# Optimization experiments

Measured on AMD Instinct MI355X. Metric: run time of the kernel, lower is better.

## Reference

```python
import jax, jax.numpy as jnp
import numpy as np

B, N, D, H = 4, 2048, 1024, 16
HD = D // H          # head dim before LRPE doubling
CHUNK = 64
BASE = 10000.0
EPS = 1e-6


def setup_inputs() -> dict:
    key = jax.random.key(0)
    ks = jax.random.split(key, 8)
    s = 0.02
    return {
        "x": jax.random.normal(ks[0], (B, N, D), jnp.float32),
        "Wq": jax.random.normal(ks[1], (D, D), jnp.float32) * s,
        "Wk": jax.random.normal(ks[2], (D, D), jnp.float32) * s,
        "Wv": jax.random.normal(ks[3], (D, D), jnp.float32) * s,
        "Wo": jax.random.normal(ks[4], (D, D), jnp.float32) * s,
        "Wg1": jax.random.normal(ks[5], (D, H), jnp.float32) * s,
        "Wg2": jax.random.normal(ks[6], (H, D), jnp.float32) * s,
        "norm_w": jnp.ones((D,), jnp.float32),
    }


def _lrpe(x, theta):
    # cosine LRPE (lrpe_type=6): d -> 2d, concat([x*cos, x*sin])
    c = jnp.cos(theta)[None, :, None, :]
    s = jnp.sin(theta)[None, :, None, :]
    return jnp.concatenate([x * c, x * s], axis=-1)


def _chunk_gla(q, k, v, g):
    # GLA chunked scan: S_t = diag(exp(g_t)) S_{t-1} + k_t^T v_t ; o_t = q_t S_t
    # q,k,g: (b,n,h,dk), v: (b,n,h,dv)
    b, n, h, dk = q.shape
    dv = v.shape[-1]
    nc = n // CHUNK

    def to_chunks(t):
        return t.reshape(b, nc, CHUNK, t.shape[2], t.shape[3]).transpose(1, 0, 2, 3, 4)

    qc, kc, vc, gc = map(to_chunks, (q, k, v, g))  # (nc,b,C,h,*)
    mask = jnp.tril(jnp.ones((CHUNK, CHUNK), bool))

    def step(S, inp):
        qi, ki, vi, gi = inp                      # (b,C,h,dk/dv)
        G = jnp.cumsum(gi, axis=1)                # inclusive cumsum of log decay
        q_g = qi * jnp.exp(G)
        k_g = ki * jnp.exp(-G)
        o_inter = jnp.einsum('bchk,bhkv->bchv', q_g, S)
        A = jnp.einsum('bchk,bshk->bhcs', q_g, k_g)
        A = jnp.where(mask[None, None], A, 0.0)
        o_intra = jnp.einsum('bhcs,bshv->bchv', A, vi)
        G_last = G[:, -1:]                        # (b,1,h,dk)
        S = S * jnp.exp(G_last[:, 0])[..., None] + jnp.einsum(
            'bchk,bchv->bhkv', ki * jnp.exp(G_last - G), vi)
        return S, o_inter + o_intra

    S0 = jnp.zeros((b, h, dk, dv), q.dtype)
    _, o = jax.lax.scan(step, S0, (qc, kc, vc, gc))
    return o.transpose(1, 0, 2, 3, 4).reshape(b, n, h, dv)


def reference(x, Wq, Wk, Wv, Wo, Wg1, Wg2, norm_w):
    b, n, d = x.shape
    q = jax.nn.silu(x @ Wq).reshape(b, n, H, HD)
    k_raw = (x @ Wk).reshape(b, n, H, HD)
    v = (x @ Wv).reshape(b, n, H, HD)

    # log-space cumulative decay from raw k projection (scalar_decay=False path)
    f = jnp.concatenate([jnp.zeros((b, 1, H, HD), jnp.float32),
                         k_raw.astype(jnp.float32)], axis=1)
    z = jax.lax.cumlogsumexp(f, axis=1)           # (b,n+1,H,HD)
    log_f = z[:, :-1] - z[:, 1:]                  # per-step log decay (<=0)
    k = jnp.exp(k_raw - z[:, 1:])                 # normalized keys

    # cosine LRPE: angles (n,HD), doubles head dim
    theta = jnp.arange(n, dtype=jnp.float32)[:, None] * \
        (BASE ** (-2.0 * jnp.arange(HD, dtype=jnp.float32) / HD))[None]
    q = _lrpe(q, theta)
    k = _lrpe(k, theta)
    g = jnp.concatenate([log_f, log_f], axis=-1)  # repeat '... d -> ... (2 d)'

    o = _chunk_gla(q, k, v, g)                    # (b,n,H,HD)
    o = o.reshape(b, n, d)

    gate = jax.nn.sigmoid((x @ Wg1) @ Wg2)        # low-rank output gate
    o = o * gate
    o = o * jax.lax.rsqrt(jnp.mean(o * o, axis=-1, keepdims=True) + EPS) * norm_w
    return o @ Wo
```

## Files before the change

kernel.cpp:

```cpp
#include <hip/hip_runtime.h>
#include <hip/hip_bf16.h>
#include <math.h>

#define B_ 4
#define N_ 2048
#define D_ 1024
#define H_ 16
#define HD_ 64

typedef __attribute__((ext_vector_type(8))) short bf16x8;
typedef __attribute__((ext_vector_type(8))) unsigned short u16x8;
typedef __attribute__((ext_vector_type(4))) float f32x4;

#define AS1(p) ((const __attribute__((address_space(1))) void*)(p))
#define AS3(p) ((__attribute__((address_space(3))) void*)(p))

__device__ inline float bf2f(unsigned short u) { return __uint_as_float(((unsigned)u) << 16); }
__device__ inline unsigned short f2bf(float f) {
  unsigned u = __float_as_uint(f);
  return (unsigned short)((u + 0x7fffu + ((u >> 16) & 1u)) >> 16);
}
__device__ inline unsigned short f2h(float f) {
  _Float16 h = (_Float16)f; unsigned short u; __builtin_memcpy(&u, &h, 2); return u;
}
__device__ inline float h2f(unsigned short u) {
  _Float16 h; __builtin_memcpy(&h, &u, 2); return (float)h;
}
__device__ inline float lseop_fast(float a, float b) {
  float mx = fmaxf(a, b), mn = fminf(a, b);
  return mx + __logf(1.f + __expf(mn - mx));
}

__global__ __launch_bounds__(256) void cast_x_bf16(const float* __restrict__ x,
                                                   unsigned short* __restrict__ xb) {
  const int t = blockIdx.x * 256 + threadIdx.x;
  float4 a = ((const float4*)x)[(size_t)t * 2];
  float4 b = ((const float4*)x)[(size_t)t * 2 + 1];
  union { unsigned short u[8]; uint4 q; } pk;
  pk.u[0] = f2bf(a.x); pk.u[1] = f2bf(a.y); pk.u[2] = f2bf(a.z); pk.u[3] = f2bf(a.w);
  pk.u[4] = f2bf(b.x); pk.u[5] = f2bf(b.y); pk.u[6] = f2bf(b.z); pk.u[7] = f2bf(b.w);
  ((uint4*)xb)[t] = pk.q;
}

__global__ __launch_bounds__(256) void cast_w_all(
    const float* __restrict__ Wq, const float* __restrict__ Wk,
    const float* __restrict__ Wv, const float* __restrict__ Wo,
    unsigned short* __restrict__ Wqkv_p, unsigned short* __restrict__ Wo_p) {
  const int bid = blockIdx.x;
  const int which = bid >> 9;
  const float* W = (which == 0) ? Wq : (which == 1) ? Wk : (which == 2) ? Wv : Wo;
  const int col0 = (which == 1) ? 1024 : (which == 2) ? 2048 : 0;
  const int Ntot = (which == 3) ? 1024 : 3072;
  unsigned short* dst = (which == 3) ? Wo_p : Wqkv_p;
  const int t = (bid & 511) * 256 + threadIdx.x;
  const int kg = t >> 10, n = t & 1023;
  union { unsigned short u[8]; uint4 q; } pk;
#pragma unroll
  for (int r = 0; r < 8; ++r)
    pk.u[r] = f2bf(W[(size_t)(kg * 8 + r) * 1024 + n]);
  *(uint4*)&dst[((size_t)kg * Ntot + col0 + n) * 8] = pk.q;
}

__global__ __launch_bounds__(256) void pack_wg1(const float* __restrict__ Wg1,
                                                unsigned short* __restrict__ Wp) {
  const int t = blockIdx.x * 256 + threadIdx.x;
  const int kg = t >> 4, hh = t & 15;
  union { unsigned short us[8]; u16x8 v; } pk;
#pragma unroll
  for (int r = 0; r < 8; ++r)
    pk.us[r] = f2bf(Wg1[(size_t)(kg * 8 + r) * 16 + hh]);
  *(u16x8*)&Wp[((size_t)kg * 16 + hh) * 8] = pk.v;
}

__global__ __launch_bounds__(256) void gate_logits(
    const unsigned short* __restrict__ x_bf, const unsigned short* __restrict__ Wg1p,
    float* __restrict__ tg) {
  __shared__ unsigned short Wl[128 * 16 * 8];
  const int tid = threadIdx.x;
  const int lane = tid & 63, w = tid >> 6;
  const int lr = lane & 15, lg = lane >> 4;
#pragma unroll
  for (int u = 0; u < 8; ++u) {
    const int flat = u * 256 + tid;
    *(u16x8*)&Wl[flat * 8] = *(const u16x8*)&Wg1p[(size_t)flat * 8];
  }
  __syncthreads();
  const int row = blockIdx.x * 64 + w * 16 + lr;
  f32x4 acc = (f32x4){0.f, 0.f, 0.f, 0.f};
  for (int ks = 0; ks < 32; ++ks) {
    bf16x8 a = *(const bf16x8*)&x_bf[(size_t)row * 1024 + ks * 32 + lg * 8];
    bf16x8 b = *(const bf16x8*)&Wl[((ks * 4 + lg) * 16 + lr) * 8];
    acc = __builtin_amdgcn_mfma_f32_16x16x32_bf16(a, b, acc, 0, 0, 0);
  }
  const int orow = blockIdx.x * 64 + w * 16 + 4 * lg;
#pragma unroll
  for (int reg = 0; reg < 4; ++reg)
    tg[(size_t)(orow + reg) * 16 + lr] = acc[reg];
}

__global__ __launch_bounds__(256) void rope_fill(float* __restrict__ ropeT) {
  const int t = blockIdx.x * 256 + threadIdx.x;
  const int n = t >> 6, hd = t & 63;
  const float freq = expf((float)hd * -0.28782313662425575f);
  float s, c;
  sincosf((float)n * freq, &s, &c);
  ropeT[(size_t)n * 128 + hd] = c;
  ropeT[(size_t)n * 128 + 64 + hd] = s;
}

__global__ __launch_bounds__(256) void gemm_qkv(
    const unsigned short* __restrict__ A, const unsigned short* __restrict__ Wp,
    unsigned short* __restrict__ qb, unsigned short* __restrict__ kh,
    unsigned short* __restrict__ vb, float* __restrict__ T, int M, int K) {
  const int Nn = 3072;
  __shared__ unsigned short Asm[2][128 * 32];
  __shared__ unsigned short Bsm[2][4 * 128 * 8];

  const int tid = threadIdx.x;
  const int lane = tid & 63;
  const int w = tid >> 6;
  const int nb = Nn >> 7;
  const int nwg = gridDim.x;
  const int cpx = nwg >> 3;
  int bid = blockIdx.x;
  bid = (bid & 7) * cpx + (bid >> 3);
  const int by = bid / nb, bx = bid % nb;
  const int m0 = by * 128, n0 = bx * 128;
  const int wr = w >> 1, wc = w & 1;

  f32x4 acc[4][4];
#pragma unroll
  for (int i = 0; i < 4; ++i)
#pragma unroll
    for (int j = 0; j < 4; ++j) acc[i][j] = (f32x4){0.f, 0.f, 0.f, 0.f};

  const int rA0 = w * 16 + (lane >> 2);
  const int rA1 = (w + 4) * 16 + (lane >> 2);
  const int sA0 = (lane & 3) ^ ((rA0 >> 1) & 3);
  const int sA1 = (lane & 3) ^ ((rA1 >> 1) & 3);
  const unsigned short* gA0 = A + (size_t)(m0 + rA0) * K + sA0 * 8;
  const unsigned short* gA1 = A + (size_t)(m0 + rA1) * K + sA1 * 8;
  const unsigned short* gB0 = Wp + (size_t)(w >> 1) * Nn * 8 +
                              (size_t)(n0 + (w & 1) * 64 + lane) * 8;
  const unsigned short* gB1 = Wp + (size_t)((w + 4) >> 1) * Nn * 8 +
                              (size_t)(n0 + ((w + 4) & 1) * 64 + lane) * 8;

  int offA[4], offB[4];
#pragma unroll
  for (int m = 0; m < 4; ++m) {
    const int rowf = wr * 64 + m * 16 + (lane & 15);
    const int sp = (lane >> 4) ^ ((rowf >> 1) & 3);
    offA[m] = rowf * 32 + sp * 8;
  }
#pragma unroll
  for (int n = 0; n < 4; ++n) {
    const int colf = wc * 64 + n * 16 + (lane & 15);
    offB[n] = (lane >> 4) * 1024 + colf * 8;
  }

  auto STAGE = [&](int buf, int t) {
    const int kt = t * 32;
    const size_t kB = (size_t)(kt >> 3) * Nn * 8;
    __builtin_amdgcn_global_load_lds(AS1(gA0 + kt), AS3(&Asm[buf][w * 512]), 16, 0, 0);
    __builtin_amdgcn_global_load_lds(AS1(gA1 + kt), AS3(&Asm[buf][(w + 4) * 512]), 16, 0, 0);
    __builtin_amdgcn_global_load_lds(AS1(gB0 + kB), AS3(&Bsm[buf][w * 512]), 16, 0, 0);
    __builtin_amdgcn_global_load_lds(AS1(gB1 + kB), AS3(&Bsm[buf][(w + 4) * 512]), 16, 0, 0);
  };

  const int NT = K >> 5;
  STAGE(0, 0);
  __syncthreads();
  int cur = 0;
  for (int t = 0; t < NT; ++t) {
    if (t + 1 < NT) STAGE(cur ^ 1, t + 1);
    bf16x8 af[4], bfr[4];
#pragma unroll
    for (int m = 0; m < 4; ++m) af[m] = *(const bf16x8*)&Asm[cur][offA[m]];
#pragma unroll
    for (int n = 0; n < 4; ++n) bfr[n] = *(const bf16x8*)&Bsm[cur][offB[n]];
#pragma unroll
    for (int m = 0; m < 4; ++m)
#pragma unroll
      for (int n = 0; n < 4; ++n)
        acc[m][n] = __builtin_amdgcn_mfma_f32_16x16x32_bf16(af[m], bfr[n], acc[m][n], 0, 0, 0);
    __syncthreads();
    cur ^= 1;
  }

  const int crow = (lane >> 4) * 4;
  const int ccol = lane & 15;
  const int slice = bx >> 3;
  if (slice == 1) {
#pragma unroll
    for (int n = 0; n < 4; ++n) {
      float se = 0.f;
#pragma unroll
      for (int m = 0; m < 4; ++m)
#pragma unroll
        for (int r = 0; r < 4; ++r) {
          float vv = acc[m][n][r];
          se += __expf(vv);
          kh[(size_t)(m0 + wr * 64 + m * 16 + crow + r) * 1024 +
             (n0 & 1023) + wc * 64 + n * 16 + ccol] = f2h(vv);
        }
      se += __shfl_xor(se, 16);
      se += __shfl_xor(se, 32);
      if ((lane >> 4) == 0) {
        const int bb = m0 >> 11;
        const int h = ((n0 & 1023) + wc * 64) >> 6;
        const int hd = n * 16 + ccol;
        const int c = ((m0 & 2047) >> 6) + wr;
        T[(size_t)((bb * 16 + h) * 64 + hd) * 32 + c] = __logf(se);
      }
    }
  } else {
#pragma unroll
    for (int m = 0; m < 4; ++m)
#pragma unroll
      for (int n = 0; n < 4; ++n)
#pragma unroll
        for (int r = 0; r < 4; ++r) {
          float vv = acc[m][n][r];
          const size_t idx = (size_t)(m0 + wr * 64 + m * 16 + crow + r) * 1024 +
                             (n0 & 1023) + wc * 64 + n * 16 + ccol;
          if (slice == 0) {
            vv = vv / (1.f + __expf(-vv));
            qb[idx] = f2bf(vv);
          } else {
            vb[idx] = f2bf(vv);
          }
        }
  }
}

__global__ __launch_bounds__(256) void gemm_bf16(
    const unsigned short* __restrict__ A, const unsigned short* __restrict__ Wp,
    float* __restrict__ Cf, int M, int K, int Nn) {
  __shared__ unsigned short Asm[2][128 * 32];
  __shared__ unsigned short Bsm[2][4 * 128 * 8];

  const int tid = threadIdx.x;
  const int lane = tid & 63;
  const int w = tid >> 6;
  const int nb = Nn >> 7;
  const int nwg = gridDim.x;
  const int cpx = nwg >> 3;
  int bid = blockIdx.x;
  bid = (bid & 7) * cpx + (bid >> 3);
  const int by = bid / nb, bx = bid % nb;
  const int m0 = by * 128, n0 = bx * 128;
  const int wr = w >> 1, wc = w & 1;

  f32x4 acc[4][4];
#pragma unroll
  for (int i = 0; i < 4; ++i)
#pragma unroll
    for (int j = 0; j < 4; ++j) acc[i][j] = (f32x4){0.f, 0.f, 0.f, 0.f};

  const int rA0 = w * 16 + (lane >> 2);
  const int rA1 = (w + 4) * 16 + (lane >> 2);
  const int sA0 = (lane & 3) ^ ((rA0 >> 1) & 3);
  const int sA1 = (lane & 3) ^ ((rA1 >> 1) & 3);
  const unsigned short* gA0 = A + (size_t)(m0 + rA0) * K + sA0 * 8;
  const unsigned short* gA1 = A + (size_t)(m0 + rA1) * K + sA1 * 8;
  const unsigned short* gB0 = Wp + (size_t)(w >> 1) * Nn * 8 +
                              (size_t)(n0 + (w & 1) * 64 + lane) * 8;
  const unsigned short* gB1 = Wp + (size_t)((w + 4) >> 1) * Nn * 8 +
                              (size_t)(n0 + ((w + 4) & 1) * 64 + lane) * 8;

  int offA[4], offB[4];
#pragma unroll
  for (int m = 0; m < 4; ++m) {
    const int rowf = wr * 64 + m * 16 + (lane & 15);
    const int sp = (lane >> 4) ^ ((rowf >> 1) & 3);
    offA[m] = rowf * 32 + sp * 8;
  }
#pragma unroll
  for (int n = 0; n < 4; ++n) {
    const int colf = wc * 64 + n * 16 + (lane & 15);
    offB[n] = (lane >> 4) * 1024 + colf * 8;
  }

  auto STAGE = [&](int buf, int t) {
    const int kt = t * 32;
    const size_t kB = (size_t)(kt >> 3) * Nn * 8;
    __builtin_amdgcn_global_load_lds(AS1(gA0 + kt), AS3(&Asm[buf][w * 512]), 16, 0, 0);
    __builtin_amdgcn_global_load_lds(AS1(gA1 + kt), AS3(&Asm[buf][(w + 4) * 512]), 16, 0, 0);
    __builtin_amdgcn_global_load_lds(AS1(gB0 + kB), AS3(&Bsm[buf][w * 512]), 16, 0, 0);
    __builtin_amdgcn_global_load_lds(AS1(gB1 + kB), AS3(&Bsm[buf][(w + 4) * 512]), 16, 0, 0);
  };

  const int NT = K >> 5;
  STAGE(0, 0);
  __syncthreads();
  int cur = 0;
  for (int t = 0; t < NT; ++t) {
    if (t + 1 < NT) STAGE(cur ^ 1, t + 1);
    bf16x8 af[4], bfr[4];
#pragma unroll
    for (int m = 0; m < 4; ++m) af[m] = *(const bf16x8*)&Asm[cur][offA[m]];
#pragma unroll
    for (int n = 0; n < 4; ++n) bfr[n] = *(const bf16x8*)&Bsm[cur][offB[n]];
#pragma unroll
    for (int m = 0; m < 4; ++m)
#pragma unroll
      for (int n = 0; n < 4; ++n)
        acc[m][n] = __builtin_amdgcn_mfma_f32_16x16x32_bf16(af[m], bfr[n], acc[m][n], 0, 0, 0);
    __syncthreads();
    cur ^= 1;
  }

  const int crow = (lane >> 4) * 4;
  const int ccol = lane & 15;
#pragma unroll
  for (int m = 0; m < 4; ++m)
#pragma unroll
    for (int n = 0; n < 4; ++n) {
#pragma unroll
      for (int r = 0; r < 4; ++r) {
        Cf[(size_t)(m0 + wr * 64 + m * 16 + crow + r) * Nn +
           n0 + wc * 64 + n * 16 + ccol] = acc[m][n][r];
      }
    }
}

__global__ void scan_pass_b(const float* __restrict__ T, float* __restrict__ Pf) {
  const int ch = blockIdx.x * 256 + threadIdx.x;
  const float* t = &T[(size_t)ch * 32];
  float* p = &Pf[(size_t)ch * 32];
  float run = 0.f;
  for (int c = 0; c < 32; ++c) {
    p[c] = run;
    run = lseop_fast(run, t[c]);
  }
}

__global__ __launch_bounds__(256) void gla_a(
    const unsigned short* __restrict__ qs, const unsigned short* __restrict__ k_h,
    const float* __restrict__ Pf, const unsigned short* __restrict__ v_bf,
    const float* __restrict__ ropeT,
    unsigned short* __restrict__ qg_p, unsigned short* __restrict__ U,
    unsigned short* __restrict__ o_bf, float* __restrict__ glast_g) {
  __shared__ unsigned short kg_l[64 * 128];
  __shared__ unsigned short kgT_l[128 * 72];
  __shared__ unsigned short vT_l[64 * 72];
  __shared__ unsigned short A_l[64 * 72];
  __shared__ unsigned short G_l[64 * 72];
  __shared__ float tot_l[4][64];
  __shared__ float glast_s[64];

  const int bid = blockIdx.x;
  const int bh = bid >> 5, c = bid & 31;
  const int b = bh >> 4, h = bh & 15;
  const int t0 = c * 64;
  const int tid = threadIdx.x;
  const int lane = tid & 63, w = tid >> 6;
  const int lr = lane & 15, lg = lane >> 4;

  const size_t qv_base = ((size_t)(b * N_ + t0) * H_ + h) * 64;

  const int jch = tid & 63, qq = tid >> 6;
  float e[16];
  {
    const float P = Pf[((size_t)bh * 64 + jch) * 32 + c];
    float psum = 0.f;
#pragma unroll
    for (int i = 0; i < 16; ++i) {
      const int r = qq * 16 + i;
      float kv = h2f(k_h[qv_base + (size_t)r * 1024 + jch]);
      float ei = __expf(kv - P);
      e[i] = ei;
      psum += ei;
      float cv = ropeT[(size_t)(t0 + r) * 128 + jch];
      float sv = ropeT[(size_t)(t0 + r) * 128 + 64 + jch];
      kg_l[r * 128 + (((jch >> 3) ^ (r & 7)) << 3) + (jch & 7)] = f2bf(ei * cv);
      kg_l[r * 128 + ((((jch + 64) >> 3) ^ (r & 7)) << 3) + (jch & 7)] = f2bf(ei * sv);
    }
    tot_l[qq][jch] = psum;
  }
  {
    const int r = tid >> 2, d0 = (tid & 3) * 16;
    u16x8 a = *(const u16x8*)&v_bf[qv_base + (size_t)r * (H_ * 64) + d0];
    u16x8 b2 = *(const u16x8*)&v_bf[qv_base + (size_t)r * (H_ * 64) + d0 + 8];
#pragma unroll
    for (int ee = 0; ee < 8; ++ee) {
      vT_l[(d0 + ee) * 72 + r] = a[ee];
      vT_l[(d0 + 8 + ee) * 72 + r] = b2[ee];
    }
  }
  __syncthreads();
  {
    float off = 0.f;
    for (int p = 0; p < qq; ++p) off += tot_l[p][jch];
    float S = off;
#pragma unroll
    for (int i = 0; i < 16; ++i) {
      S += e[i];
      G_l[(qq * 16 + i) * 72 + jch] = f2h(-__logf(1.f + S));
    }
    if (qq == 3) {
      glast_g[(size_t)bid * 64 + jch] = -__logf(1.f + S);
      glast_s[jch] = 1.f / (1.f + S);
    }
  }
  {
    const int j = tid >> 1, sh = (tid & 1) * 32;
#pragma unroll
    for (int u = 0; u < 4; ++u) {
      union { unsigned short us[8]; u16x8 v; } tv;
#pragma unroll
      for (int ee = 0; ee < 8; ++ee) {
        const int s = sh + 8 * u + ee;
        tv.us[ee] = kg_l[s * 128 + (((j >> 3) ^ (s & 7)) * 8) + (j & 7)];
      }
      *(u16x8*)&kgT_l[j * 72 + sh + 8 * u] = tv.v;
    }
  }
  __syncthreads();

  bf16x8 af[4];
  {
    const int r = 16 * w + lr;
#pragma unroll
    for (int ks = 0; ks < 4; ++ks) {
      const int jb = 32 * ks + 8 * lg;
      const int jq = jb & 63;
      u16x8 q8 = *(const u16x8*)&qs[qv_base + (size_t)r * (H_ * 64) + jq];
      u16x8 gh8 = *(const u16x8*)&G_l[r * 72 + jq];
      float4 r0 = *(const float4*)&ropeT[(size_t)(t0 + r) * 128 + jb];
      float4 r1 = *(const float4*)&ropeT[(size_t)(t0 + r) * 128 + jb + 4];
      float rr[8] = {r0.x, r0.y, r0.z, r0.w, r1.x, r1.y, r1.z, r1.w};
      union { unsigned short us[8]; bf16x8 v; u16x8 uv; } pk;
#pragma unroll
      for (int ee = 0; ee < 8; ++ee)
        pk.us[ee] = f2bf(bf2f(q8[ee]) * rr[ee] * __expf(h2f(gh8[ee])));
      af[ks] = pk.v;
      *(u16x8*)&qg_p[((((size_t)bid * 4 + w) * 4 + ks) * 64 + lane) * 8] = pk.uv;
    }
  }
  f32x4 acc1[4];
#pragma unroll
  for (int n = 0; n < 4; ++n) acc1[n] = (f32x4){0.f, 0.f, 0.f, 0.f};
#pragma unroll
  for (int n = 0; n < 4; ++n) {
    const int s = 16 * n + lr;
#pragma unroll
    for (int ks = 0; ks < 4; ++ks) {
      bf16x8 bk = *(const bf16x8*)&kg_l[s * 128 + (((lg + 4 * ks) ^ (s & 7)) * 8)];
      acc1[n] = __builtin_amdgcn_mfma_f32_16x16x32_bf16(af[ks], bk, acc1[n], 0, 0, 0);
    }
  }
#pragma unroll
  for (int n = 0; n < 4; ++n) {
    const int s = 16 * n + lr;
#pragma unroll
    for (int reg = 0; reg < 4; ++reg) {
      const int cr = 16 * w + 4 * lg + reg;
      A_l[cr * 72 + s] = (s <= cr) ? f2bf(acc1[n][reg]) : (unsigned short)0;
    }
  }
  f32x4 acc2[8];
#pragma unroll
  for (int n = 0; n < 8; ++n) acc2[n] = (f32x4){0.f, 0.f, 0.f, 0.f};
#pragma unroll
  for (int ks = 0; ks < 2; ++ks) {
    const int s0 = 32 * ks + 8 * lg;
    bf16x8 av = *(const bf16x8*)&vT_l[(16 * w + lr) * 72 + s0];
#pragma unroll
    for (int n = 0; n < 8; ++n) {
      bf16x8 bk = *(const bf16x8*)&kgT_l[(16 * n + lr) * 72 + s0];
      acc2[n] = __builtin_amdgcn_mfma_f32_16x16x32_bf16(av, bk, acc2[n], 0, 0, 0);
    }
  }
  __syncthreads();
  float es[4];
#pragma unroll
  for (int n = 0; n < 4; ++n) es[n] = glast_s[16 * n + lr];
#pragma unroll
  for (int n = 0; n < 8; ++n) {
    const int j = 16 * n + lr;
    const float ee = es[n & 3];
#pragma unroll
    for (int reg = 0; reg < 4; ++reg)
      kg_l[(16 * w + 4 * lg + reg) * 128 + j] = f2bf(acc2[n][reg] * ee);
  }
  f32x4 acc3[4];
#pragma unroll
  for (int n = 0; n < 4; ++n) acc3[n] = (f32x4){0.f, 0.f, 0.f, 0.f};
#pragma unroll
  for (int ks = 0; ks < 2; ++ks) {
    const int s0 = 32 * ks + 8 * lg;
    bf16x8 aA = *(const bf16x8*)&A_l[(16 * w + lr) * 72 + s0];
#pragma unroll
    for (int n = 0; n < 4; ++n) {
      bf16x8 bV = *(const bf16x8*)&vT_l[(16 * n + lr) * 72 + s0];
      acc3[n] = __builtin_amdgcn_mfma_f32_16x16x32_bf16(aA, bV, acc3[n], 0, 0, 0);
    }
  }
#pragma unroll
  for (int n = 0; n < 4; ++n)
#pragma unroll
    for (int reg = 0; reg < 4; ++reg)
      o_bf[qv_base + (size_t)(16 * w + 4 * lg + reg) * (H_ * 64) + 16 * n + lr] =
          f2bf(acc3[n][reg]);
  __syncthreads();
#pragma unroll
  for (int u = 0; u < 4; ++u) {
    const int flat = u * 256 + tid;
    const int d = flat >> 4, sl = flat & 15;
    *(u16x8*)&U[((size_t)bid * 64 + d) * 128 + sl * 8] =
        *(const u16x8*)&kg_l[d * 128 + sl * 8];
  }
}

__global__ __launch_bounds__(256) void gla_b(unsigned short* __restrict__ U,
                                             const float* __restrict__ glast_g) {
  const int t = blockIdx.x * 256 + threadIdx.x;
  const int j4 = t & 31;
  const int d = (t >> 5) & 63;
  const int bh = t >> 11;
  const int jj0 = (4 * j4) & 63;
  float s0 = 0.f, s1 = 0.f, s2 = 0.f, s3 = 0.f;
  for (int c = 0; c < 32; ++c) {
    const size_t ub = ((size_t)((bh * 32 + c) * 64 + d)) * 128 + 4 * j4;
    ushort4 uv = *(const ushort4*)&U[ub];
    float4 g4 = *(const float4*)&glast_g[(size_t)(bh * 32 + c) * 64 + jj0];
    ushort4 pv;
    pv.x = f2bf(s0); pv.y = f2bf(s1); pv.z = f2bf(s2); pv.w = f2bf(s3);
    *(ushort4*)&U[ub] = pv;
    s0 = s0 * __expf(g4.x) + bf2f(uv.x);
    s1 = s1 * __expf(g4.y) + bf2f(uv.y);
    s2 = s2 * __expf(g4.z) + bf2f(uv.z);
    s3 = s3 * __expf(g4.w) + bf2f(uv.w);
  }
}

__global__ __launch_bounds__(256) void gla_c(
    const unsigned short* __restrict__ qg_p, const unsigned short* __restrict__ S,
    unsigned short* __restrict__ o_bf) {
  __shared__ unsigned short S_l[64 * 128];
  const int bid = blockIdx.x;
  const int bh = bid >> 5, c = bid & 31;
  const int b = bh >> 4, h = bh & 15;
  const int t0 = c * 64;
  const int tid = threadIdx.x;
  const int lane = tid & 63, w = tid >> 6;
  const int lr = lane & 15, lg = lane >> 4;
  const size_t s_base = (size_t)bid * 64 * 128;
  const size_t o_base = ((size_t)(b * N_ + t0) * H_ + h) * 64;

#pragma unroll
  for (int u = 0; u < 4; ++u) {
    const int flat = u * 256 + tid;
    const int d = flat >> 4, sl = flat & 15;
    u16x8 src = *(const u16x8*)&S[s_base + (size_t)d * 128 + sl * 8];
    *(u16x8*)&S_l[d * 128 + ((sl ^ (d & 7)) * 8)] = src;
  }
  __syncthreads();
  bf16x8 af[4];
#pragma unroll
  for (int ks = 0; ks < 4; ++ks)
    af[ks] = *(const bf16x8*)&qg_p[((((size_t)bid * 4 + w) * 4 + ks) * 64 + lane) * 8];
  f32x4 acc[4];
#pragma unroll
  for (int n = 0; n < 4; ++n) acc[n] = (f32x4){0.f, 0.f, 0.f, 0.f};
#pragma unroll
  for (int n = 0; n < 4; ++n) {
    const int d = 16 * n + lr;
#pragma unroll
    for (int ks = 0; ks < 4; ++ks) {
      bf16x8 bk = *(const bf16x8*)&S_l[d * 128 + (((lg + 4 * ks) ^ (d & 7)) * 8)];
      acc[n] = __builtin_amdgcn_mfma_f32_16x16x32_bf16(af[ks], bk, acc[n], 0, 0, 0);
    }
  }
#pragma unroll
  for (int n = 0; n < 4; ++n)
#pragma unroll
    for (int reg = 0; reg < 4; ++reg) {
      const size_t idx = o_base + (size_t)(16 * w + 4 * lg + reg) * (H_ * 64) + 16 * n + lr;
      o_bf[idx] = f2bf(bf2f(o_bf[idx]) + acc[n][reg]);
    }
}

__global__ __launch_bounds__(256) void gate_norm2(
    const float* __restrict__ tg, const float* __restrict__ Wg2,
    const float* __restrict__ nw, const unsigned short* __restrict__ o_bf,
    unsigned short* __restrict__ og) {
  const int w = threadIdx.x >> 6, lane = threadIdx.x & 63;
  const int row = blockIdx.x * 4 + w;
  float tgv[16];
  const float* tp = &tg[(size_t)row * 16];
#pragma unroll
  for (int hh = 0; hh < 16; ++hh) tgv[hh] = tp[hh];
  float ogr[4][4];
  float ssq = 0.f;
#pragma unroll
  for (int u = 0; u < 4; ++u) {
    const int d0 = u * 256 + lane * 4;
    ushort4 o4 = *(const ushort4*)&o_bf[(size_t)row * 1024 + d0];
    float oa[4] = {bf2f(o4.x), bf2f(o4.y), bf2f(o4.z), bf2f(o4.w)};
    float sgx = 0.f, sgy = 0.f, sgz = 0.f, sgw = 0.f;
#pragma unroll
    for (int hh = 0; hh < 16; ++hh) {
      float4 w4 = *(const float4*)&Wg2[hh * 1024 + d0];
      sgx += tgv[hh] * w4.x; sgy += tgv[hh] * w4.y;
      sgz += tgv[hh] * w4.z; sgw += tgv[hh] * w4.w;
    }
    ogr[u][0] = oa[0] / (1.f + __expf(-sgx));
    ogr[u][1] = oa[1] / (1.f + __expf(-sgy));
    ogr[u][2] = oa[2] / (1.f + __expf(-sgz));
    ogr[u][3] = oa[3] / (1.f + __expf(-sgw));
    ssq += ogr[u][0] * ogr[u][0] + ogr[u][1] * ogr[u][1] +
           ogr[u][2] * ogr[u][2] + ogr[u][3] * ogr[u][3];
  }
#pragma unroll
  for (int off = 32; off > 0; off >>= 1) ssq += __shfl_xor(ssq, off);
  const float rinv = rsqrtf(ssq * (1.f / 1024.f) + 1e-6f);
#pragma unroll
  for (int u = 0; u < 4; ++u) {
    const int d0 = u * 256 + lane * 4;
    float4 nw4 = *(const float4*)&nw[d0];
    ushort4 st;
    st.x = f2bf(ogr[u][0] * rinv * nw4.x);
    st.y = f2bf(ogr[u][1] * rinv * nw4.y);
    st.z = f2bf(ogr[u][2] * rinv * nw4.z);
    st.w = f2bf(ogr[u][3] * rinv * nw4.w);
    *(ushort4*)&og[(size_t)row * 1024 + d0] = st;
  }
}

extern "C" void kernel_launch(void* const* d_in, const int* in_sizes, int n_in,
                              void* d_out, int out_size, void* d_ws, size_t ws_size,
                              hipStream_t stream) {
  const float* x   = (const float*)d_in[0];
  const float* Wq  = (const float*)d_in[1];
  const float* Wk  = (const float*)d_in[2];
  const float* Wv  = (const float*)d_in[3];
  const float* Wo  = (const float*)d_in[4];
  const float* Wg1 = (const float*)d_in[5];
  const float* Wg2 = (const float*)d_in[6];
  const float* nw  = (const float*)d_in[7];
  float* out = (float*)d_out;
  float* ws  = (float*)d_ws;

  const size_t P = (size_t)B_ * N_ * D_;
  unsigned short* k_h = (unsigned short*)ws;
  unsigned short* o_bf = (unsigned short*)(ws + P);
  unsigned short* qg_p = (unsigned short*)(ws + 3 * P);
  unsigned short* U_buf = (unsigned short*)(ws + 4 * P);
  unsigned short* v_bf = (unsigned short*)(ws + 5 * P);
  unsigned short* q_bf = (unsigned short*)(ws + 5 * P + P / 2);
  float* ropeT = ws + 6 * P;
  float* T_buf = ws + 6 * P + 524288;
  float* P_buf = T_buf + 131072;
  unsigned short* Wg1p = (unsigned short*)(ws + 6 * P + 786432);
  float* tg_buf = ws + 6 * P + 794624;
  unsigned short* x_bf = (unsigned short*)(ws + 13 * P / 2);
  unsigned short* og_bf = x_bf;
  unsigned short* Wqkv_p = (unsigned short*)(ws + 7 * P);
  unsigned short* Wo_p = (unsigned short*)(ws + 7 * P + 1572864);
  float* glast_g = ws + 7 * P + 2097152;

  const int M = B_ * N_;
  const int ggrid = (M / 128) * (D_ / 128);
  const int qkvgrid = (M / 128) * (3 * D_ / 128);

  cast_x_bf16<<<(int)(P / 2048), 256, 0, stream>>>(x, x_bf);
  rope_fill<<<512, 256, 0, stream>>>(ropeT);
  cast_w_all<<<2048, 256, 0, stream>>>(Wq, Wk, Wv, Wo, Wqkv_p, Wo_p);
  pack_wg1<<<8, 256, 0, stream>>>(Wg1, Wg1p);
  gate_logits<<<M / 64, 256, 0, stream>>>(x_bf, Wg1p, tg_buf);
  gemm_qkv<<<qkvgrid, 256, 0, stream>>>(x_bf, Wqkv_p, q_bf, k_h, v_bf, T_buf, M, D_);
  scan_pass_b<<<16, 256, 0, stream>>>(T_buf, P_buf);
  gla_a<<<2048, 256, 0, stream>>>(q_bf, k_h, P_buf, v_bf, ropeT, qg_p, U_buf, o_bf, glast_g);
  gla_b<<<512, 256, 0, stream>>>(U_buf, glast_g);
  gla_c<<<2048, 256, 0, stream>>>(qg_p, U_buf, o_bf);
  gate_norm2<<<M / 4, 256, 0, stream>>>(tg_buf, Wg2, nw, o_bf, og_bf);
  gemm_bf16<<<ggrid, 256, 0, stream>>>(og_bf, Wo_p, out, M, D_, D_);
}
```

Before: 214.9 us.

## Fuse gate-logit projection into QKV GEMM and triple-buffer GEMM main loops

Wg1 is packed as 16 extra columns of the QKV weight matrix, padded to 3200 columns, so the separate gate_logits kernel is removed. Gate logits now come from an extra column tile in gemm_qkv. Both the QKV and output GEMMs move from double to triple LDS buffering, with explicit vmcnt waits and raw barriers so global-to-LDS loads run two stages ahead. This saves one launch and one extra pass over x, at the cost of a mostly wasted padded tile column (112 of 128 columns unused) and more LDS per block, which may lower occupancy.

```diff
diff --git a/kernel.cpp b/kernel.cpp
--- a/kernel.cpp
+++ b/kernel.cpp
@@ -50,7 +50,7 @@
   const int which = bid >> 9;
   const float* W = (which == 0) ? Wq : (which == 1) ? Wk : (which == 2) ? Wv : Wo;
   const int col0 = (which == 1) ? 1024 : (which == 2) ? 2048 : 0;
-  const int Ntot = (which == 3) ? 1024 : 3072;
+  const int Ntot = (which == 3) ? 1024 : 3200;
   unsigned short* dst = (which == 3) ? Wo_p : Wqkv_p;
   const int t = (bid & 511) * 256 + threadIdx.x;
   const int kg = t >> 10, n = t & 1023;
@@ -62,40 +62,14 @@
 }
 
 __global__ __launch_bounds__(256) void pack_wg1(const float* __restrict__ Wg1,
-                                                unsigned short* __restrict__ Wp) {
+                                                unsigned short* __restrict__ Wqkv_p) {
   const int t = blockIdx.x * 256 + threadIdx.x;
   const int kg = t >> 4, hh = t & 15;
   union { unsigned short us[8]; u16x8 v; } pk;
 #pragma unroll
   for (int r = 0; r < 8; ++r)
     pk.us[r] = f2bf(Wg1[(size_t)(kg * 8 + r) * 16 + hh]);
-  *(u16x8*)&Wp[((size_t)kg * 16 + hh) * 8] = pk.v;
-}
-
-__global__ __launch_bounds__(256) void gate_logits(
-    const unsigned short* __restrict__ x_bf, const unsigned short* __restrict__ Wg1p,
-    float* __restrict__ tg) {
-  __shared__ unsigned short Wl[128 * 16 * 8];
-  const int tid = threadIdx.x;
-  const int lane = tid & 63, w = tid >> 6;
-  const int lr = lane & 15, lg = lane >> 4;
-#pragma unroll
-  for (int u = 0; u < 8; ++u) {
-    const int flat = u * 256 + tid;
-    *(u16x8*)&Wl[flat * 8] = *(const u16x8*)&Wg1p[(size_t)flat * 8];
-  }
-  __syncthreads();
-  const int row = blockIdx.x * 64 + w * 16 + lr;
-  f32x4 acc = (f32x4){0.f, 0.f, 0.f, 0.f};
-  for (int ks = 0; ks < 32; ++ks) {
-    bf16x8 a = *(const bf16x8*)&x_bf[(size_t)row * 1024 + ks * 32 + lg * 8];
-    bf16x8 b = *(const bf16x8*)&Wl[((ks * 4 + lg) * 16 + lr) * 8];
-    acc = __builtin_amdgcn_mfma_f32_16x16x32_bf16(a, b, acc, 0, 0, 0);
-  }
-  const int orow = blockIdx.x * 64 + w * 16 + 4 * lg;
-#pragma unroll
-  for (int reg = 0; reg < 4; ++reg)
-    tg[(size_t)(orow + reg) * 16 + lr] = acc[reg];
+  *(u16x8*)&Wqkv_p[((size_t)kg * 3200 + 3072 + hh) * 8] = pk.v;
 }
 
 __global__ __launch_bounds__(256) void rope_fill(float* __restrict__ ropeT) {
@@ -111,15 +85,16 @@
 __global__ __launch_bounds__(256) void gemm_qkv(
     const unsigned short* __restrict__ A, const unsigned short* __restrict__ Wp,
     unsigned short* __restrict__ qb, unsigned short* __restrict__ kh,
-    unsigned short* __restrict__ vb, float* __restrict__ T, int M, int K) {
-  const int Nn = 3072;
-  __shared__ unsigned short Asm[2][128 * 32];
-  __shared__ unsigned short Bsm[2][4 * 128 * 8];
+    unsigned short* __restrict__ vb, float* __restrict__ T,
+    float* __restrict__ tg, int M, int K) {
+  const int Nn = 3200;
+  __shared__ unsigned short Asm[3][128 * 32];
+  __shared__ unsigned short Bsm[3][4 * 128 * 8];
 
   const int tid = threadIdx.x;
   const int lane = tid & 63;
   const int w = tid >> 6;
-  const int nb = Nn >> 7;
+  const int nb = 25;
   const int nwg = gridDim.x;
   const int cpx = nwg >> 3;
   int bid = blockIdx.x;
@@ -166,26 +141,38 @@
     __builtin_amdgcn_global_load_lds(AS1(gB0 + kB), AS3(&Bsm[buf][w * 512]), 16, 0, 0);
     __builtin_amdgcn_global_load_lds(AS1(gB1 + kB), AS3(&Bsm[buf][(w + 4) * 512]), 16, 0, 0);
   };
+  auto COMPUTE = [&](int buf) {
+    bf16x8 af[4], bfr[4];
+#pragma unroll
+    for (int m = 0; m < 4; ++m) af[m] = *(const bf16x8*)&Asm[buf][offA[m]];
+#pragma unroll
+    for (int n = 0; n < 4; ++n) bfr[n] = *(const bf16x8*)&Bsm[buf][offB[n]];
+#pragma unroll
+    for (int m = 0; m < 4; ++m)
+#pragma unroll
+      for (int n = 0; n < 4; ++n)
+        acc[m][n] = __builtin_amdgcn_mfma_f32_16x16x32_bf16(af[m], bfr[n], acc[m][n], 0, 0, 0);
+  };
 
   const int NT = K >> 5;
   STAGE(0, 0);
-  __syncthreads();
+  STAGE(1, 1);
   int cur = 0;
-  for (int t = 0; t < NT; ++t) {
-    if (t + 1 < NT) STAGE(cur ^ 1, t + 1);
-    bf16x8 af[4], bfr[4];
-#pragma unroll
-    for (int m = 0; m < 4; ++m) af[m] = *(const bf16x8*)&Asm[cur][offA[m]];
-#pragma unroll
-    for (int n = 0; n < 4; ++n) bfr[n] = *(const bf16x8*)&Bsm[cur][offB[n]];
-#pragma unroll
-    for (int m = 0; m < 4; ++m)
-#pragma unroll
-      for (int n = 0; n < 4; ++n)
-        acc[m][n] = __builtin_amdgcn_mfma_f32_16x16x32_bf16(af[m], bfr[n], acc[m][n], 0, 0, 0);
-    __syncthreads();
-    cur ^= 1;
-  }
+  for (int t = 0; t < NT - 1; ++t) {
+    asm volatile("s_waitcnt vmcnt(4)" ::: "memory");
+    __builtin_amdgcn_s_barrier();
+    __builtin_amdgcn_sched_barrier(0);
+    if (t + 2 < NT) {
+      int nx = cur + 2; if (nx >= 3) nx -= 3;
+      STAGE(nx, t + 2);
+    }
+    COMPUTE(cur);
+    cur = (cur + 1 < 3) ? cur + 1 : 0;
+  }
+  asm volatile("s_waitcnt vmcnt(0)" ::: "memory");
+  __builtin_amdgcn_s_barrier();
+  __builtin_amdgcn_sched_barrier(0);
+  COMPUTE(cur);
 
   const int crow = (lane >> 4) * 4;
   const int ccol = lane & 15;
@@ -213,6 +200,14 @@
         T[(size_t)((bb * 16 + h) * 64 + hd) * 32 + c] = __logf(se);
       }
     }
+  } else if (slice == 3) {
+    if (wc == 0) {
+#pragma unroll
+      for (int m = 0; m < 4; ++m)
+#pragma unroll
+        for (int r = 0; r < 4; ++r)
+          tg[(size_t)(m0 + wr * 64 + m * 16 + crow + r) * 16 + ccol] = acc[m][0][r];
+    }
   } else {
 #pragma unroll
     for (int m = 0; m < 4; ++m)
@@ -236,8 +231,8 @@
 __global__ __launch_bounds__(256) void gemm_bf16(
     const unsigned short* __restrict__ A, const unsigned short* __restrict__ Wp,
     float* __restrict__ Cf, int M, int K, int Nn) {
-  __shared__ unsigned short Asm[2][128 * 32];
-  __shared__ unsigned short Bsm[2][4 * 128 * 8];
+  __shared__ unsigned short Asm[3][128 * 32];
+  __shared__ unsigned short Bsm[3][4 * 128 * 8];
 
   const int tid = threadIdx.x;
   const int lane = tid & 63;
@@ -289,26 +284,38 @@
     __builtin_amdgcn_global_load_lds(AS1(gB0 + kB), AS3(&Bsm[buf][w * 512]), 16, 0, 0);
     __builtin_amdgcn_global_load_lds(AS1(gB1 + kB), AS3(&Bsm[buf][(w + 4) * 512]), 16, 0, 0);
   };
+  auto COMPUTE = [&](int buf) {
+    bf16x8 af[4], bfr[4];
+#pragma unroll
+    for (int m = 0; m < 4; ++m) af[m] = *(const bf16x8*)&Asm[buf][offA[m]];
+#pragma unroll
+    for (int n = 0; n < 4; ++n) bfr[n] = *(const bf16x8*)&Bsm[buf][offB[n]];
+#pragma unroll
+    for (int m = 0; m < 4; ++m)
+#pragma unroll
+      for (int n = 0; n < 4; ++n)
+        acc[m][n] = __builtin_amdgcn_mfma_f32_16x16x32_bf16(af[m], bfr[n], acc[m][n], 0, 0, 0);
+  };
 
   const int NT = K >> 5;
   STAGE(0, 0);
-  __syncthreads();
+  STAGE(1, 1);
   int cur = 0;
-  for (int t = 0; t < NT; ++t) {
-    if (t + 1 < NT) STAGE(cur ^ 1, t + 1);
-    bf16x8 af[4], bfr[4];
-#pragma unroll
-    for (int m = 0; m < 4; ++m) af[m] = *(const bf16x8*)&Asm[cur][offA[m]];
-#pragma unroll
-    for (int n = 0; n < 4; ++n) bfr[n] = *(const bf16x8*)&Bsm[cur][offB[n]];
-#pragma unroll
-    for (int m = 0; m < 4; ++m)
-#pragma unroll
-      for (int n = 0; n < 4; ++n)
-        acc[m][n] = __builtin_amdgcn_mfma_f32_16x16x32_bf16(af[m], bfr[n], acc[m][n], 0, 0, 0);
-    __syncthreads();
-    cur ^= 1;
-  }
+  for (int t = 0; t < NT - 1; ++t) {
+    asm volatile("s_waitcnt vmcnt(4)" ::: "memory");
+    __builtin_amdgcn_s_barrier();
+    __builtin_amdgcn_sched_barrier(0);
+    if (t + 2 < NT) {
+      int nx = cur + 2; if (nx >= 3) nx -= 3;
+      STAGE(nx, t + 2);
+    }
+    COMPUTE(cur);
+    cur = (cur + 1 < 3) ? cur + 1 : 0;
+  }
+  asm volatile("s_waitcnt vmcnt(0)" ::: "memory");
+  __builtin_amdgcn_s_barrier();
+  __builtin_amdgcn_sched_barrier(0);
+  COMPUTE(cur);
 
   const int crow = (lane >> 4) * 4;
   const int ccol = lane & 15;
@@ -653,24 +660,22 @@
   float* ropeT = ws + 6 * P;
   float* T_buf = ws + 6 * P + 524288;
   float* P_buf = T_buf + 131072;
-  unsigned short* Wg1p = (unsigned short*)(ws + 6 * P + 786432);
   float* tg_buf = ws + 6 * P + 794624;
   unsigned short* x_bf = (unsigned short*)(ws + 13 * P / 2);
   unsigned short* og_bf = x_bf;
   unsigned short* Wqkv_p = (unsigned short*)(ws + 7 * P);
-  unsigned short* Wo_p = (unsigned short*)(ws + 7 * P + 1572864);
-  float* glast_g = ws + 7 * P + 2097152;
+  unsigned short* Wo_p = (unsigned short*)(ws + 7 * P + 1638400);
+  float* glast_g = ws + 7 * P + 1638400 + 524288;
 
   const int M = B_ * N_;
   const int ggrid = (M / 128) * (D_ / 128);
-  const int qkvgrid = (M / 128) * (3 * D_ / 128);
+  const int qkvgrid = (M / 128) * 25;
 
   cast_x_bf16<<<(int)(P / 2048), 256, 0, stream>>>(x, x_bf);
   rope_fill<<<512, 256, 0, stream>>>(ropeT);
   cast_w_all<<<2048, 256, 0, stream>>>(Wq, Wk, Wv, Wo, Wqkv_p, Wo_p);
-  pack_wg1<<<8, 256, 0, stream>>>(Wg1, Wg1p);
-  gate_logits<<<M / 64, 256, 0, stream>>>(x_bf, Wg1p, tg_buf);
-  gemm_qkv<<<qkvgrid, 256, 0, stream>>>(x_bf, Wqkv_p, q_bf, k_h, v_bf, T_buf, M, D_);
+  pack_wg1<<<8, 256, 0, stream>>>(Wg1, Wqkv_p);
+  gemm_qkv<<<qkvgrid, 256, 0, stream>>>(x_bf, Wqkv_p, q_bf, k_h, v_bf, T_buf, tg_buf, M, D_);
   scan_pass_b<<<16, 256, 0, stream>>>(T_buf, P_buf);
   gla_a<<<2048, 256, 0, stream>>>(q_bf, k_h, P_buf, v_bf, ropeT, qg_p, U_buf, o_bf, glast_g);
   gla_b<<<512, 256, 0, stream>>>(U_buf, glast_g);
```

Result: slower. 223.4 us (+3.9%).
